# Kernel tuning notes

Measured on AMD Instinct MI355X. Metric: run time of the kernel, lower is better.

Reference implementation:

```python
import jax, jax.numpy as jnp
import numpy as np

NF, IN_NF, N_LAYERS = 64, 196, 3
B, H, W = 1, 256, 256
P3 = [(1, 1), (1, 1)]
P1 = [(0, 0), (0, 0)]


def conv2d(x, w, pad):
    return jax.lax.conv_general_dilated(x, w, (1, 1), pad,
                                        dimension_numbers=('NCHW', 'OIHW', 'NCHW'))


def prelu(x, a):
    return jnp.where(x >= 0, x, a[None, :, None, None] * x)


def warp(x, flow):
    # standard backward bilinear warp, zero padding outside the image
    Bx, C, Hx, Wx = x.shape
    yy, xx = jnp.meshgrid(jnp.arange(Hx, dtype=x.dtype),
                          jnp.arange(Wx, dtype=x.dtype), indexing='ij')
    px = xx[None] + flow[:, 0]  # (B,H,W)
    py = yy[None] + flow[:, 1]

    def sample(img, px, py):  # img (C,H,W); px,py (H,W)
        x0 = jnp.floor(px)
        y0 = jnp.floor(py)
        x1 = x0 + 1.0
        y1 = y0 + 1.0
        wx1 = px - x0
        wx0 = 1.0 - wx1
        wy1 = py - y0
        wy0 = 1.0 - wy1

        def gather(xi, yi):
            valid = (xi >= 0) & (xi <= Wx - 1) & (yi >= 0) & (yi <= Hx - 1)
            xc = jnp.clip(xi, 0, Wx - 1).astype(jnp.int32)
            yc = jnp.clip(yi, 0, Hx - 1).astype(jnp.int32)
            return img[:, yc, xc] * valid.astype(img.dtype)

        return (gather(x0, y0) * (wx0 * wy0) + gather(x1, y0) * (wx1 * wy0)
                + gather(x0, y1) * (wx0 * wy1) + gather(x1, y1) * (wx1 * wy1))

    return jax.vmap(sample)(x, px, py)


def setup_inputs() -> dict:
    key = jax.random.key(0)
    ks = jax.random.split(key, 11)
    s = 0.05
    return {
        'feat_0': jax.random.normal(ks[0], (B, 64, H, W), jnp.float32),
        'feat_1': jax.random.normal(ks[1], (B, 64, H, W), jnp.float32),
        'feat_dense': jax.random.normal(ks[2], (B, 64, H, W), jnp.float32),
        'flow': jax.random.normal(ks[3], (B, 4, H, W), jnp.float32),
        'space_mask': jax.random.uniform(ks[4], (B, 1, H, W), jnp.float32),
        'head_w': jax.random.normal(ks[5], (IN_NF, IN_NF, 3, 3), jnp.float32) * s,
        'head_a': jnp.full((IN_NF,), 0.25, jnp.float32),
        'conv_w': jax.random.normal(ks[6], (N_LAYERS, IN_NF, IN_NF, 3, 3), jnp.float32) * s,
        'conv_a': jnp.full((N_LAYERS, IN_NF), 0.25, jnp.float32),
        'last_w': jax.random.normal(ks[7], (4 + NF, IN_NF * (N_LAYERS + 1), 1, 1), jnp.float32) * s,
        'last_b': jax.random.normal(ks[8], (4 + NF,), jnp.float32) * s,
        'mask_w': jax.random.normal(ks[9], (2, NF, 3, 3), jnp.float32) * s,
        'mask_b': jax.random.normal(ks[10], (2,), jnp.float32) * s,
    }


def reference(feat_0, feat_1, feat_dense, flow, space_mask,
              head_w, head_a, conv_w, conv_a, last_w, last_b, mask_w, mask_b):
    f0 = warp(feat_0, flow[:, :2])
    f1 = warp(feat_1, flow[:, 2:4])
    x = jnp.concatenate([f0, f1, feat_dense, flow], axis=1)  # (B, in_nf, H, W)
    sm_up = jnp.repeat(jnp.repeat(space_mask, 2, axis=2), 2, axis=3)

    # head: conv3x3 -> PReLU, then mask (dense / use_sparsity=False path)
    x = prelu(conv2d(x, head_w, P3), head_a) * space_mask
    outs = [x]
    for i in range(N_LAYERS):
        x = conv2d(x, conv_w[i], P3) * space_mask
        x = prelu(x, conv_a[i])
        outs.append(x)
    x = conv2d(jnp.concatenate(outs, axis=1), last_w, P1) + last_b[None, :, None, None]

    smn = conv2d(x[:, 4:], mask_w, P3) + mask_b[None, :, None, None]

    Bx, Cx, Hx, Wx = x.shape
    x_up = jax.image.resize(x, (Bx, Cx, 2 * Hx, 2 * Wx), method='bilinear')
    smn_up = jax.image.resize(smn, (Bx, 2, 2 * Hx, 2 * Wx), method='bilinear')

    flow_out = x_up[:, :4]
    feat_t = x_up[:, 4:]
    # eval-mode mask (training=False): hard argmax between channel 0 and 1
    mask_next = (smn_up[:, :1] > smn_up[:, 1:2]).astype(x.dtype) * sm_up
    return flow_out, feat_t, mask_next
```

## Files before the change

kernel.cpp:

```cpp
#include <hip/hip_runtime.h>

typedef _Float16 f16;
typedef _Float16 f16x8 __attribute__((ext_vector_type(8)));
typedef _Float16 f16x4 __attribute__((ext_vector_type(4)));
typedef float    f32x4 __attribute__((ext_vector_type(4)));
typedef float    f32x16 __attribute__((ext_vector_type(16)));

#define MFMA16(a,b,c) __builtin_amdgcn_mfma_f32_16x16x32_f16(a,b,c,0,0,0)
#define MFMA32(a,b,c) __builtin_amdgcn_mfma_f32_32x32x16_f16(a,b,c,0,0,0)

#define NPIX 65536
#define PXS   8
#define KHS   2064
#define K16S  4128
#define HS    8256
#define CBS   16512
#define ROWH  115584
#define RBYTES 231168
#define SBUF  ((size_t)258*RBYTES)

#define PKSUB  7168
#define PK_CONV 903168
#define NMICRO 117

#define PKL_CB  5120
#define PKL_BI  35840

#define ASTG 14336
#define BSTG 16640

__global__ void k_pack_conv(const float* __restrict__ head_w,
                            const float* __restrict__ conv_w,
                            f16* __restrict__ dst)
{
    int t = blockIdx.x*256 + threadIdx.x;
    int lane = t & 63; t >>= 6;
    int ob  = t % 7;  t /= 7;
    int sel = t & 1;  t >>= 1;
    int kx  = t % 3;  t /= 3;
    int k16 = t & 1;  t >>= 1;
    int cb  = t % 7;  t /= 7;
    int ky  = t % 3;  t /= 3;
    int li  = t;
    if (li >= 4) return;
    if (cb == 6 && k16 == 1) return;
    const float* W = (li == 0) ? head_w : (conv_w + (size_t)(li-1)*196*196*9);
    int oc  = ob*32 + (lane & 31);
    int ic0 = cb*32 + k16*16 + (lane >> 5)*8;
    int tap = ky*3 + kx;
    f16x8 v;
#pragma unroll
    for (int j = 0; j < 8; ++j) {
        int ic = ic0 + j;
        float x = 0.f;
        if (oc < 196 && ic < 196) x = W[((size_t)oc*196 + ic)*9 + tap];
        f16 h = (f16)x;
        v[j] = (sel == 0) ? h : (f16)(x - (float)h);
    }
    int pos = ky*39 + ((cb < 6) ? (cb*6 + k16*3 + kx) : (36 + kx));
    *(f16x8*)(dst + (size_t)li*PK_CONV + (size_t)pos*PKSUB
              + (size_t)(sel*7 + ob)*512 + (size_t)lane*8) = v;
}

__global__ void k_pack_last(const float* __restrict__ last_w, f16* __restrict__ dst)
{
    int t = blockIdx.x*256 + threadIdx.x;
    if (t >= 4*7*5*2*64) return;
    int lane = t & 63; t >>= 6;
    int sel  = t & 1;  t >>= 1;
    int ob   = t % 5;  t /= 5;
    int cb   = t % 7;  t /= 7;
    int bi   = t;
    int oc = ob*16 + (lane & 15);
    int k0 = cb*32 + (lane >> 4)*8;
    f16x8 v;
#pragma unroll
    for (int j = 0; j < 8; ++j) {
        int k = k0 + j;
        float x = 0.f;
        if (oc < 68 && k < 196) x = last_w[(size_t)oc*784 + bi*196 + k];
        f16 h = (f16)x;
        v[j] = (sel == 0) ? h : (f16)(x - (float)h);
    }
    *(f16x8*)(dst + (((size_t)((bi*7+cb)*5 + ob)*2 + sel)*64 + lane)*8) = v;
}

__global__ void k_zero_halo(f16* __restrict__ bufA, f16* __restrict__ bufB)
{
    int c = blockIdx.x*256 + threadIdx.x;
    int end = c & 1; c >>= 1;
    int kh  = c & 1; c >>= 1;
    int k16 = c & 1; c >>= 1;
    int h   = c & 1; c >>= 1;
    int cb  = c % 7; c /= 7;
    int row = c % 258; c /= 258;
    if (c >= 2) return;
    f16* base = (c == 0) ? bufA : bufB;
    f16* p = base + (size_t)row*ROWH + cb*CBS + h*HS + k16*K16S + kh*KHS + (end ? 257 : 0)*PXS;
    f16x8 z = {(f16)0,(f16)0,(f16)0,(f16)0,(f16)0,(f16)0,(f16)0,(f16)0};
    *(f16x8*)p = z;
}

struct Gath { int o00,o01,o10,o11; float w00,w01,w10,w11; };

__device__ inline Gath mk_gath(float pxf, float pyf)
{
    float x0 = floorf(pxf), y0 = floorf(pyf);
    float x1 = x0 + 1.f, y1 = y0 + 1.f;
    float wx1 = pxf - x0, wx0 = 1.f - wx1;
    float wy1 = pyf - y0, wy0 = 1.f - wy1;
    bool vx0 = (x0 >= 0.f) && (x0 <= 255.f);
    bool vx1 = (x1 >= 0.f) && (x1 <= 255.f);
    bool vy0 = (y0 >= 0.f) && (y0 <= 255.f);
    bool vy1 = (y1 >= 0.f) && (y1 <= 255.f);
    int ix0 = min(max((int)x0, 0), 255);
    int ix1 = min(max((int)x1, 0), 255);
    int iy0 = min(max((int)y0, 0), 255);
    int iy1 = min(max((int)y1, 0), 255);
    Gath g;
    g.o00 = iy0*256 + ix0; g.w00 = (vx0 && vy0) ? wx0*wy0 : 0.f;
    g.o01 = iy0*256 + ix1; g.w01 = (vx1 && vy0) ? wx1*wy0 : 0.f;
    g.o10 = iy1*256 + ix0; g.w10 = (vx0 && vy1) ? wx0*wy1 : 0.f;
    g.o11 = iy1*256 + ix1; g.w11 = (vx1 && vy1) ? wx1*wy1 : 0.f;
    return g;
}

__device__ inline void store4n(f16* __restrict__ rowb, int slot, int c0,
                               float a, float b, float c, float d)
{
    f16x4 hi, lo;
    f16 h;
    h = (f16)a; hi[0] = h; lo[0] = (f16)(a - (float)h);
    h = (f16)b; hi[1] = h; lo[1] = (f16)(b - (float)h);
    h = (f16)c; hi[2] = h; lo[2] = (f16)(c - (float)h);
    h = (f16)d; hi[3] = h; lo[3] = (f16)(d - (float)h);
    int cb = c0 >> 5, w32 = c0 & 31;
    f16* p = rowb + cb*CBS + (w32 >> 4)*K16S + ((w32 >> 3) & 1)*KHS
                 + (size_t)slot*PXS + (w32 & 7);
    *(f16x4*)p        = hi;
    *(f16x4*)(p + HS) = lo;
}

__global__ void k_warp_concat(const float* __restrict__ f0, const float* __restrict__ f1,
                              const float* __restrict__ fd, const float* __restrict__ flow,
                              f16* __restrict__ out)
{
    int px = blockIdx.x*256 + threadIdx.x;
    int row = px >> 8, col = px & 255;
    f16* rowb = out + (size_t)(row+1)*ROWH;
    int slot = col + 1;
    Gath g0 = mk_gath((float)col + flow[px],          (float)row + flow[NPIX   + px]);
    Gath g1 = mk_gath((float)col + flow[2*NPIX + px], (float)row + flow[3*NPIX + px]);
#pragma unroll
    for (int c = 0; c < 64; c += 4) {
        float v[4];
#pragma unroll
        for (int r = 0; r < 4; ++r) {
            const float* im = f0 + (size_t)(c+r)*NPIX;
            v[r] = g0.w00*im[g0.o00] + g0.w01*im[g0.o01] + g0.w10*im[g0.o10] + g0.w11*im[g0.o11];
        }
        store4n(rowb, slot, c, v[0], v[1], v[2], v[3]);
    }
#pragma unroll
    for (int c = 0; c < 64; c += 4) {
        float v[4];
#pragma unroll
        for (int r = 0; r < 4; ++r) {
            const float* im = f1 + (size_t)(c+r)*NPIX;
            v[r] = g1.w00*im[g1.o00] + g1.w01*im[g1.o01] + g1.w10*im[g1.o10] + g1.w11*im[g1.o11];
        }
        store4n(rowb, slot, 64 + c, v[0], v[1], v[2], v[3]);
    }
#pragma unroll
    for (int c = 0; c < 64; c += 4) {
        store4n(rowb, slot, 128 + c, fd[(size_t)(c+0)*NPIX + px], fd[(size_t)(c+1)*NPIX + px],
                                     fd[(size_t)(c+2)*NPIX + px], fd[(size_t)(c+3)*NPIX + px]);
    }
    store4n(rowb, slot, 192, flow[px], flow[NPIX+px], flow[2*NPIX+px], flow[3*NPIX+px]);
#pragma unroll
    for (int c = 196; c < 224; c += 4) store4n(rowb, slot, c, 0.f, 0.f, 0.f, 0.f);
}

template<int NOB, int OB0>
__device__ __forceinline__ void micro(const char* __restrict__ ab, const char* __restrict__ bl,
                                      f32x16 (&acc)[4][2], int lane)
{
    f16x8 Bh[2], Bl[2];
    Bh[0] = *(const f16x8*)(bl);
    Bh[1] = *(const f16x8*)(bl + 512);
    Bl[0] = *(const f16x8*)(bl + 8320);
    Bl[1] = *(const f16x8*)(bl + 8320 + 512);
#pragma unroll
    for (int o = 0; o < NOB; ++o) {
        f16x8 Ah = *(const f16x8*)(ab + (OB0 + o)*1024 + lane*16);
        f16x8 Al = *(const f16x8*)(ab + (7 + OB0 + o)*1024 + lane*16);
#pragma unroll
        for (int pt = 0; pt < 2; ++pt) {
            acc[o][pt] = MFMA32(Ah, Bh[pt], acc[o][pt]);
            acc[o][pt] = MFMA32(Al, Bh[pt], acc[o][pt]);
            acc[o][pt] = MFMA32(Ah, Bl[pt], acc[o][pt]);
        }
    }
}

__global__ __launch_bounds__(256, 2)
void k_conv32(const f16* __restrict__ in, f16* __restrict__ out,
              const f16* __restrict__ pack, const float* __restrict__ alpha,
              const float* __restrict__ mask)
{
    __shared__ __align__(16) char As[3][ASTG];
    __shared__ __align__(16) char Bs[2][BSTG];

    int bid = blockIdx.x;
    int wg  = (bid & 7)*64 + (bid >> 3);
    int row  = wg >> 1;
    int half = wg & 1;
    int tid  = threadIdx.x;
    int lane = tid & 63;
    int w    = tid >> 6;
    int ocg  = ((w >> 1) ^ bid) & 1;
    int pxg  = w & 1;
    int l31 = lane & 31, lk = lane >> 5;
    int cb0 = half*128;

    f32x16 acc[4][2];
#pragma unroll
    for (int o = 0; o < 4; ++o)
#pragma unroll
        for (int pt = 0; pt < 2; ++pt)
#pragma unroll
            for (int e = 0; e < 16; ++e) acc[o][pt][e] = 0.f;

    auto stageA = [&](int b, const f16* src) {
        __builtin_amdgcn_global_load_lds(
            (const __attribute__((address_space(1))) void*)(src + (size_t)tid*8),
            (__attribute__((address_space(3))) void*)(&As[b][0] + tid*16), 16, 0, 0);
        __builtin_amdgcn_global_load_lds(
            (const __attribute__((address_space(1))) void*)(src + (size_t)(tid+256)*8),
            (__attribute__((address_space(3))) void*)(&As[b][0] + (tid+256)*16), 16, 0, 0);
        __builtin_amdgcn_global_load_lds(
            (const __attribute__((address_space(1))) void*)(src + (size_t)(tid+512)*8),
            (__attribute__((address_space(3))) void*)(&As[b][0] + (tid+512)*16), 16, 0, 0);
        if (tid < 128)
            __builtin_amdgcn_global_load_lds(
                (const __attribute__((address_space(1))) void*)(src + (size_t)(tid+768)*8),
                (__attribute__((address_space(3))) void*)(&As[b][0] + (tid+768)*16), 16, 0, 0);
    };

    auto stageB = [&](int b, const f16* g) {
#pragma unroll
        for (int u = 0; u < 5; ++u) {
            int c = tid + u*256;
            if (u < 4 || c < 1040) {
                int pl = c / 130;
                int i  = c - pl*130;
                const f16* src = g + (size_t)pl*KHS + (size_t)(cb0 + i)*PXS;
                __builtin_amdgcn_global_load_lds(
                    (const __attribute__((address_space(1))) void*)src,
                    (__attribute__((address_space(3))) void*)(&Bs[b][0] + c*16),
                    16, 0, 0);
            }
        }
    };

    const int lbase = lk*2080 + (pxg*64 + l31)*16;

    const f16* g = in + (size_t)row*ROWH;
    stageB(0, g);
    stageA(0, pack);
    stageA(1, pack + PKSUB);
    __syncthreads();

    int bsel = 0;
    int q = 0;
    for (int ky = 0; ky < 3; ++ky) {
        for (int cb = 0; cb < 7; ++cb) {
            int nk16 = (cb == 6) ? 1 : 2;
            bool lastPhase = (ky == 2) && (cb == 6);
            if (!lastPhase) {
                const f16* gn = (cb < 6) ? (g + CBS) : (g + ROWH - 6*CBS);
                stageB(bsel ^ 1, gn);
                g = gn;
            }
            for (int k16 = 0; k16 < nk16; ++k16) {
#pragma unroll
                for (int kx = 0; kx < 3; ++kx) {
                    if (q + 2 < NMICRO) {
                        int nb = q + 2;
                        stageA(nb - (nb/3)*3, pack + (size_t)nb*PKSUB);
                    }
                    const char* ab = &As[q - (q/3)*3][0];
                    const char* bl = &Bs[bsel][0] + lbase + k16*4160 + kx*16;
                    __builtin_amdgcn_s_setprio(1);
                    if (ocg == 0) micro<4,0>(ab, bl, acc, lane);
                    else          micro<3,4>(ab, bl, acc, lane);
                    __builtin_amdgcn_s_setprio(0);
                    __syncthreads();
                    ++q;
                }
            }
            bsel ^= 1;
        }
    }

    int nob = (ocg == 0) ? 4 : 3;
    int ob0 = (ocg == 0) ? 0 : 4;
    int colbase = cb0 + pxg*64;
    float mv[2];
#pragma unroll
    for (int pt = 0; pt < 2; ++pt) mv[pt] = mask[row*256 + colbase + pt*32 + l31];
#pragma unroll
    for (int o = 0; o < 4; ++o) {
        if (o >= nob) continue;
        int ob = ob0 + o;
#pragma unroll
        for (int qg = 0; qg < 4; ++qg) {
            int oc0 = ob*32 + 8*qg + 4*lk;
            f32x4 a4 = *(const f32x4*)(alpha + min(oc0, 192));
#pragma unroll
            for (int pt = 0; pt < 2; ++pt) {
                f16x4 hi, lo;
#pragma unroll
                for (int e = 0; e < 4; ++e) {
                    float v = acc[o][pt][qg*4 + e];
                    v = (v >= 0.f ? v : a4[e]*v) * mv[pt];
                    f16 h = (f16)v;
                    hi[e] = h;
                    lo[e] = (f16)(v - (float)h);
                }
                f16* p = out + (size_t)(row+1)*ROWH + (size_t)(colbase + pt*32 + l31 + 1)*PXS
                       + lk*4 + ob*CBS + (qg >> 1)*K16S + (qg & 1)*KHS;
                *(f16x4*)p        = hi;
                *(f16x4*)(p + HS) = lo;
            }
        }
    }
}

__global__ __launch_bounds__(256, 4)
void k_acc_last(const f16* __restrict__ in, const f16* __restrict__ pack,
                const float* __restrict__ bias, float* __restrict__ accp, int bi)
{
    int lane = threadIdx.x & 63;
    int wid  = (blockIdx.x << 2) | (threadIdx.x >> 6);
    int row  = wid >> 3;
    int col0 = (wid & 7) << 5;
    int l15 = lane & 15, lk = lane >> 4;

    f32x4 acc[5][2];
#pragma unroll
    for (int i = 0; i < 5; ++i)
#pragma unroll
        for (int j = 0; j < 2; ++j)
            acc[i][j] = (f32x4){0.f, 0.f, 0.f, 0.f};

    const f16* bb = in + (size_t)(row+1)*ROWH + (size_t)(col0 + l15 + 1)*PXS
                  + (lk >> 1)*K16S + (lk & 1)*KHS;
    const f16* ap = pack + (size_t)bi*PKL_BI + (size_t)lane*8;
    for (int cb = 0; cb < 7; ++cb) {
        f16x8 bh[2], bl[2];
#pragma unroll
        for (int pb = 0; pb < 2; ++pb) {
            const f16* p = bb + cb*CBS + pb*16*PXS;
            bh[pb] = *(const f16x8*)p;
            bl[pb] = *(const f16x8*)(p + HS);
        }
        const f16* a = ap + cb*PKL_CB;
#pragma unroll
        for (int ob = 0; ob < 5; ++ob) {
            f16x8 ah = *(const f16x8*)(a + ob*1024);
            f16x8 al = *(const f16x8*)(a + ob*1024 + 512);
#pragma unroll
            for (int pb = 0; pb < 2; ++pb) {
                acc[ob][pb] = MFMA16(ah, bh[pb], acc[ob][pb]);
                acc[ob][pb] = MFMA16(ah, bl[pb], acc[ob][pb]);
                acc[ob][pb] = MFMA16(al, bh[pb], acc[ob][pb]);
            }
        }
    }
#pragma unroll
    for (int ob = 0; ob < 5; ++ob) {
        int oc0 = ob*16 + lk*4;
        if (oc0 >= 72) continue;
#pragma unroll
        for (int pb = 0; pb < 2; ++pb) {
            int px = row*256 + col0 + pb*16 + l15;
            float* dst = accp + (size_t)px*72 + oc0;
            f32x4 d = acc[ob][pb];
            if (bi == 0) {
                f32x4 b4;
#pragma unroll
                for (int r = 0; r < 4; ++r) b4[r] = bias[min(oc0 + r, 67)];
                *(f32x4*)dst = d + b4;
            } else {
                *(f32x4*)dst = *(const f32x4*)dst + d;
            }
        }
    }
}

__global__ void k_smn(const float* __restrict__ accp, const float* __restrict__ mw,
                      const float* __restrict__ mb, float* __restrict__ smn)
{
    int px = blockIdx.x*256 + threadIdx.x;
    int row = px >> 8, col = px & 255;
    float s0 = mb[0], s1 = mb[1];
    for (int ky = 0; ky < 3; ++ky) {
        int r = row + ky - 1;
        if ((unsigned)r > 255u) continue;
        for (int kx = 0; kx < 3; ++kx) {
            int c = col + kx - 1;
            if ((unsigned)c > 255u) continue;
            const float* ab = accp + ((size_t)r*256 + c)*72 + 4;
            const float* w  = mw + ky*3 + kx;
#pragma unroll
            for (int ch = 0; ch < 64; ch += 4) {
                f32x4 v = *(const f32x4*)(ab + ch);
                s0 += v[0]*w[(ch+0)*9] + v[1]*w[(ch+1)*9] + v[2]*w[(ch+2)*9] + v[3]*w[(ch+3)*9];
                s1 += v[0]*w[(64+ch+0)*9] + v[1]*w[(64+ch+1)*9] + v[2]*w[(64+ch+2)*9] + v[3]*w[(64+ch+3)*9];
            }
        }
    }
    smn[px]        = s0;
    smn[NPIX + px] = s1;
}

__global__ void k_upsample(const float* __restrict__ accp, float* __restrict__ outp)
{
    int o = blockIdx.x*256 + threadIdx.x;
    int oy = o >> 9, ox = o & 511;
    int my = oy >> 1, mx = ox >> 1;
    int r0, r1, c0, c1; float wy0, wy1, wx0, wx1;
    if (oy & 1) { r0 = my;            r1 = min(my+1, 255); wy0 = 0.75f; wy1 = 0.25f; }
    else        { r0 = max(my-1, 0);  r1 = my;             wy0 = 0.25f; wy1 = 0.75f; }
    if (ox & 1) { c0 = mx;            c1 = min(mx+1, 255); wx0 = 0.75f; wx1 = 0.25f; }
    else        { c0 = max(mx-1, 0);  c1 = mx;             wx0 = 0.25f; wx1 = 0.75f; }
    const float* p00 = accp + ((size_t)r0*256 + c0)*72;
    const float* p01 = accp + ((size_t)r0*256 + c1)*72;
    const float* p10 = accp + ((size_t)r1*256 + c0)*72;
    const float* p11 = accp + ((size_t)r1*256 + c1)*72;
    float w00 = wy0*wx0, w01 = wy0*wx1, w10 = wy1*wx0, w11 = wy1*wx1;
#pragma unroll
    for (int ch = 0; ch < 68; ch += 4) {
        f32x4 va = *(const f32x4*)(p00 + ch);
        f32x4 vb = *(const f32x4*)(p01 + ch);
        f32x4 vc = *(const f32x4*)(p10 + ch);
        f32x4 vd = *(const f32x4*)(p11 + ch);
        f32x4 v;
#pragma unroll
        for (int r = 0; r < 4; ++r)
            v[r] = w00*va[r] + w01*vb[r] + w10*vc[r] + w11*vd[r];
        outp[(size_t)(ch+0)*262144 + o] = v[0];
        outp[(size_t)(ch+1)*262144 + o] = v[1];
        outp[(size_t)(ch+2)*262144 + o] = v[2];
        outp[(size_t)(ch+3)*262144 + o] = v[3];
    }
}

__global__ void k_mask(const float* __restrict__ smn, const float* __restrict__ sm,
                       float* __restrict__ outp)
{
    int o = blockIdx.x*256 + threadIdx.x;
    int oy = o >> 9, ox = o & 511;
    int my = oy >> 1, mx = ox >> 1;
    int r0, r1, c0, c1; float wy0, wy1, wx0, wx1;
    if (oy & 1) { r0 = my;            r1 = min(my+1, 255); wy0 = 0.75f; wy1 = 0.25f; }
    else        { r0 = max(my-1, 0);  r1 = my;             wy0 = 0.25f; wy1 = 0.75f; }
    if (ox & 1) { c0 = mx;            c1 = min(mx+1, 255); wx0 = 0.75f; wx1 = 0.25f; }
    else        { c0 = max(mx-1, 0);  c1 = mx;             wx0 = 0.25f; wx1 = 0.75f; }
    float w00 = wy0*wx0, w01 = wy0*wx1, w10 = wy1*wx0, w11 = wy1*wx1;
    int i00 = r0*256 + c0, i01 = r0*256 + c1, i10 = r1*256 + c0, i11 = r1*256 + c1;
    float s0 = w00*smn[i00] + w01*smn[i01] + w10*smn[i10] + w11*smn[i11];
    float s1 = w00*smn[NPIX+i00] + w01*smn[NPIX+i01] + w10*smn[NPIX+i10] + w11*smn[NPIX+i11];
    outp[(size_t)68*262144 + o] = (s0 > s1) ? sm[my*256 + mx] : 0.f;
}

extern "C" void kernel_launch(void* const* d_in, const int* in_sizes, int n_in,
                              void* d_out, int out_size, void* d_ws, size_t ws_size,
                              hipStream_t stream)
{
    const float* feat0  = (const float*)d_in[0];
    const float* feat1  = (const float*)d_in[1];
    const float* featd  = (const float*)d_in[2];
    const float* flow   = (const float*)d_in[3];
    const float* smask  = (const float*)d_in[4];
    const float* head_w = (const float*)d_in[5];
    const float* head_a = (const float*)d_in[6];
    const float* conv_w = (const float*)d_in[7];
    const float* conv_a = (const float*)d_in[8];
    const float* last_w = (const float*)d_in[9];
    const float* last_b = (const float*)d_in[10];
    const float* mask_w = (const float*)d_in[11];
    const float* mask_b = (const float*)d_in[12];
    float* outp = (float*)d_out;

    char* ws = (char*)d_ws;
    size_t off = 0;
    f16* bufA = (f16*)(ws + off); off += SBUF;
    f16* bufB = (f16*)(ws + off); off += SBUF;
    f16* packc = (f16*)(ws + off); off += (size_t)4*PK_CONV*2;
    f16* packl = (f16*)(ws + off); off += (size_t)4*PKL_BI*2;
    float* accp = (float*)(ws + off); off += (size_t)NPIX*72*4;
    float* smn  = (float*)(ws + off); off += (size_t)2*NPIX*4;

    hipMemsetAsync(bufA, 0, RBYTES, stream);
    hipMemsetAsync((char*)bufA + (size_t)257*RBYTES, 0, RBYTES, stream);
    hipMemsetAsync(bufB, 0, RBYTES, stream);
    hipMemsetAsync((char*)bufB + (size_t)257*RBYTES, 0, RBYTES, stream);
    k_zero_halo<<<226, 256, 0, stream>>>(bufA, bufB);

    k_pack_conv<<<1764, 256, 0, stream>>>(head_w, conv_w, packc);
    k_pack_last<<<70, 256, 0, stream>>>(last_w, packl);
    k_warp_concat<<<256, 256, 0, stream>>>(feat0, feat1, featd, flow, bufA);

    k_conv32<<<512, 256, 0, stream>>>(bufA, bufB, packc, head_a, smask);
    k_acc_last<<<512, 256, 0, stream>>>(bufB, packl, last_b, accp, 0);
    k_conv32<<<512, 256, 0, stream>>>(bufB, bufA, packc + (size_t)1*PK_CONV, conv_a, smask);
    k_acc_last<<<512, 256, 0, stream>>>(bufA, packl, last_b, accp, 1);
    k_conv32<<<512, 256, 0, stream>>>(bufA, bufB, packc + (size_t)2*PK_CONV, conv_a + 196, smask);
    k_acc_last<<<512, 256, 0, stream>>>(bufB, packl, last_b, accp, 2);
    k_conv32<<<512, 256, 0, stream>>>(bufB, bufA, packc + (size_t)3*PK_CONV, conv_a + 392, smask);
    k_acc_last<<<512, 256, 0, stream>>>(bufA, packl, last_b, accp, 3);

    k_smn<<<256, 256, 0, stream>>>(accp, mask_w, mask_b, smn);
    k_upsample<<<1024, 256, 0, stream>>>(accp, outp);
    k_mask<<<1024, 256, 0, stream>>>(smn, smask, outp);
}
```

Measured before the change: 804.2 us.

## Replace per-step block barriers with vmcnt waits and per-wave staging

The conv kernel is restructured so each wave stages only the weight fragments it consumes and its own pixel slice of the input tile. It uses explicit s_waitcnt vmcnt counts plus a barrier every second micro-step instead of a full __syncthreads after every step. The weight pipeline depth drops from three stages in flight to two, and the body is templated on the output-block count. The goal is to cut barrier stalls and redundant staging, but the hand-tuned vmcnt counts and the barrier skipping risk races if the wave-to-buffer ownership assumptions are wrong.

```diff
diff --git a/kernel.cpp b/kernel.cpp
--- a/kernel.cpp
+++ b/kernel.cpp
@@ -8,6 +8,10 @@
 
 #define MFMA16(a,b,c) __builtin_amdgcn_mfma_f32_16x16x32_f16(a,b,c,0,0,0)
 #define MFMA32(a,b,c) __builtin_amdgcn_mfma_f32_32x32x16_f16(a,b,c,0,0,0)
+
+#define AS1 __attribute__((address_space(1)))
+#define AS3 __attribute__((address_space(3)))
+#define WAITVM(N) asm volatile("s_waitcnt vmcnt(" #N ")" ::: "memory")
 
 #define NPIX 65536
 #define PXS   8
@@ -27,7 +31,7 @@
 #define PKL_BI  35840
 
 #define ASTG 14336
-#define BSTG 16640
+#define BSTG 17408
 
 __global__ void k_pack_conv(const float* __restrict__ head_w,
                             const float* __restrict__ conv_w,
@@ -182,137 +186,125 @@
 }
 
 template<int NOB, int OB0>
-__device__ __forceinline__ void micro(const char* __restrict__ ab, const char* __restrict__ bl,
-                                      f32x16 (&acc)[4][2], int lane)
-{
-    f16x8 Bh[2], Bl[2];
-    Bh[0] = *(const f16x8*)(bl);
-    Bh[1] = *(const f16x8*)(bl + 512);
-    Bl[0] = *(const f16x8*)(bl + 8320);
-    Bl[1] = *(const f16x8*)(bl + 8320 + 512);
-#pragma unroll
-    for (int o = 0; o < NOB; ++o) {
-        f16x8 Ah = *(const f16x8*)(ab + (OB0 + o)*1024 + lane*16);
-        f16x8 Al = *(const f16x8*)(ab + (7 + OB0 + o)*1024 + lane*16);
-#pragma unroll
-        for (int pt = 0; pt < 2; ++pt) {
-            acc[o][pt] = MFMA32(Ah, Bh[pt], acc[o][pt]);
-            acc[o][pt] = MFMA32(Al, Bh[pt], acc[o][pt]);
-            acc[o][pt] = MFMA32(Ah, Bl[pt], acc[o][pt]);
-        }
-    }
-}
-
-__global__ __launch_bounds__(256, 2)
-void k_conv32(const f16* __restrict__ in, f16* __restrict__ out,
-              const f16* __restrict__ pack, const float* __restrict__ alpha,
-              const float* __restrict__ mask)
-{
-    __shared__ __align__(16) char As[3][ASTG];
-    __shared__ __align__(16) char Bs[2][BSTG];
-
-    int bid = blockIdx.x;
-    int wg  = (bid & 7)*64 + (bid >> 3);
-    int row  = wg >> 1;
-    int half = wg & 1;
-    int tid  = threadIdx.x;
-    int lane = tid & 63;
-    int w    = tid >> 6;
-    int ocg  = ((w >> 1) ^ bid) & 1;
-    int pxg  = w & 1;
+__device__ __forceinline__ void conv_body(
+    const f16* __restrict__ in, f16* __restrict__ out,
+    const f16* __restrict__ pack, const float* __restrict__ alpha,
+    const float* __restrict__ mask,
+    char* Asb, char* Bsb, int row, int cb0, int lane, int pxg, int bid)
+{
     int l31 = lane & 31, lk = lane >> 5;
-    int cb0 = half*128;
-
-    f32x16 acc[4][2];
-#pragma unroll
-    for (int o = 0; o < 4; ++o)
+
+    f32x16 acc[NOB][2];
+#pragma unroll
+    for (int o = 0; o < NOB; ++o)
 #pragma unroll
         for (int pt = 0; pt < 2; ++pt)
 #pragma unroll
             for (int e = 0; e < 16; ++e) acc[o][pt][e] = 0.f;
 
-    auto stageA = [&](int b, const f16* src) {
+    auto stageA = [&](int b, int qi) {
+        const f16* src = pack + (size_t)qi*PKSUB;
+        char* dst = Asb + b*ASTG;
+#pragma unroll
+        for (int j = 0; j < NOB; ++j) {
+            int fr1 = OB0 + j, fr2 = 7 + OB0 + j;
+            __builtin_amdgcn_global_load_lds(
+                (const AS1 void*)(src + fr1*512 + lane*8),
+                (AS3 void*)(dst + fr1*1024 + lane*16), 16, 0, 0);
+            __builtin_amdgcn_global_load_lds(
+                (const AS1 void*)(src + fr2*512 + lane*8),
+                (AS3 void*)(dst + fr2*1024 + lane*16), 16, 0, 0);
+        }
+    };
+
+    auto stageB = [&](int b, const f16* g) {
+        char* dst = Bsb + b*BSTG;
+#pragma unroll
+        for (int u = 0; u < 8; ++u) {
+            __builtin_amdgcn_global_load_lds(
+                (const AS1 void*)(g + (size_t)u*KHS + (size_t)(cb0 + pxg*64 + lane)*PXS),
+                (AS3 void*)(dst + (u*128 + pxg*64)*16 + lane*16), 16, 0, 0);
+        }
+        int idx = lane & 15;
+        int pl  = idx >> 1;
+        int il  = idx & 1;
         __builtin_amdgcn_global_load_lds(
-            (const __attribute__((address_space(1))) void*)(src + (size_t)tid*8),
-            (__attribute__((address_space(3))) void*)(&As[b][0] + tid*16), 16, 0, 0);
-        __builtin_amdgcn_global_load_lds(
-            (const __attribute__((address_space(1))) void*)(src + (size_t)(tid+256)*8),
-            (__attribute__((address_space(3))) void*)(&As[b][0] + (tid+256)*16), 16, 0, 0);
-        __builtin_amdgcn_global_load_lds(
-            (const __attribute__((address_space(1))) void*)(src + (size_t)(tid+512)*8),
-            (__attribute__((address_space(3))) void*)(&As[b][0] + (tid+512)*16), 16, 0, 0);
-        if (tid < 128)
-            __builtin_amdgcn_global_load_lds(
-                (const __attribute__((address_space(1))) void*)(src + (size_t)(tid+768)*8),
-                (__attribute__((address_space(3))) void*)(&As[b][0] + (tid+768)*16), 16, 0, 0);
+            (const AS1 void*)(g + (size_t)pl*KHS + (size_t)(cb0 + 128 + il)*PXS),
+            (AS3 void*)(dst + 16384 + lane*16), 16, 0, 0);
     };
 
-    auto stageB = [&](int b, const f16* g) {
-#pragma unroll
-        for (int u = 0; u < 5; ++u) {
-            int c = tid + u*256;
-            if (u < 4 || c < 1040) {
-                int pl = c / 130;
-                int i  = c - pl*130;
-                const f16* src = g + (size_t)pl*KHS + (size_t)(cb0 + i)*PXS;
-                __builtin_amdgcn_global_load_lds(
-                    (const __attribute__((address_space(1))) void*)src,
-                    (__attribute__((address_space(3))) void*)(&Bs[b][0] + c*16),
-                    16, 0, 0);
-            }
-        }
+    auto bptr = [&](const char* Bb, int pl, int sl) -> const char* {
+        return (sl < 128) ? (Bb + pl*2048 + sl*16)
+                          : (Bb + 16384 + pl*32 + (sl - 128)*16);
     };
-
-    const int lbase = lk*2080 + (pxg*64 + l31)*16;
 
     const f16* g = in + (size_t)row*ROWH;
     stageB(0, g);
-    stageA(0, pack);
-    stageA(1, pack + PKSUB);
-    __syncthreads();
-
-    int bsel = 0;
-    int q = 0;
+    stageA(0, 0);
+
+    int acur = 0, bsel = 0, q = 0;
     for (int ky = 0; ky < 3; ++ky) {
         for (int cb = 0; cb < 7; ++cb) {
+            bool lastPhase = (ky == 2) && (cb == 6);
             int nk16 = (cb == 6) ? 1 : 2;
-            bool lastPhase = (ky == 2) && (cb == 6);
-            if (!lastPhase) {
-                const f16* gn = (cb < 6) ? (g + CBS) : (g + ROWH - 6*CBS);
-                stageB(bsel ^ 1, gn);
-                g = gn;
-            }
-            for (int k16 = 0; k16 < nk16; ++k16) {
+            const f16* gn = (cb < 6) ? (g + CBS) : (g + ROWH - 6*CBS);
+            for (int k16 = 0; k16 < 2; ++k16) {
+                if (k16 >= nk16) break;
 #pragma unroll
                 for (int kx = 0; kx < 3; ++kx) {
-                    if (q + 2 < NMICRO) {
-                        int nb = q + 2;
-                        stageA(nb - (nb/3)*3, pack + (size_t)nb*PKSUB);
+                    int anx = (acur == 2) ? 0 : (acur + 1);
+                    bool aload = (q + 1 < NMICRO);
+                    if (aload) stageA(anx, q + 1);
+                    if (aload) {
+                        if (k16 == 0 && kx == 1 && !lastPhase) {
+                            if (NOB == 4) WAITVM(17); else WAITVM(15);
+                        } else {
+                            if (NOB == 4) WAITVM(8);  else WAITVM(6);
+                        }
+                    } else {
+                        WAITVM(0);
                     }
-                    const char* ab = &As[q - (q/3)*3][0];
-                    const char* bl = &Bs[bsel][0] + lbase + k16*4160 + kx*16;
+                    if ((q & 1) == 0) __builtin_amdgcn_s_barrier();
+                    if (k16 == 0 && kx == 0 && !lastPhase) stageB(bsel ^ 1, gn);
+
+                    const char* ab = Asb + acur*ASTG;
+                    const char* Bb = Bsb + bsel*BSTG;
+                    f16x8 Bh[2], Bl[2];
+#pragma unroll
+                    for (int pt = 0; pt < 2; ++pt) {
+                        int sl = pxg*64 + l31 + kx + pt*32;
+                        int plh = k16*2 + lk;
+                        Bh[pt] = *(const f16x8*)bptr(Bb, plh, sl);
+                        Bl[pt] = *(const f16x8*)bptr(Bb, 4 + plh, sl);
+                    }
                     __builtin_amdgcn_s_setprio(1);
-                    if (ocg == 0) micro<4,0>(ab, bl, acc, lane);
-                    else          micro<3,4>(ab, bl, acc, lane);
+#pragma unroll
+                    for (int o = 0; o < NOB; ++o) {
+                        f16x8 Ah = *(const f16x8*)(ab + (OB0 + o)*1024 + lane*16);
+                        f16x8 Al = *(const f16x8*)(ab + (7 + OB0 + o)*1024 + lane*16);
+#pragma unroll
+                        for (int pt = 0; pt < 2; ++pt) {
+                            acc[o][pt] = MFMA32(Ah, Bh[pt], acc[o][pt]);
+                            acc[o][pt] = MFMA32(Al, Bh[pt], acc[o][pt]);
+                            acc[o][pt] = MFMA32(Ah, Bl[pt], acc[o][pt]);
+                        }
+                    }
                     __builtin_amdgcn_s_setprio(0);
-                    __syncthreads();
+                    acur = anx;
                     ++q;
                 }
             }
-            bsel ^= 1;
-        }
-    }
-
-    int nob = (ocg == 0) ? 4 : 3;
-    int ob0 = (ocg == 0) ? 0 : 4;
+            if (!lastPhase) { g = gn; bsel ^= 1; }
+        }
+    }
+
     int colbase = cb0 + pxg*64;
     float mv[2];
 #pragma unroll
     for (int pt = 0; pt < 2; ++pt) mv[pt] = mask[row*256 + colbase + pt*32 + l31];
 #pragma unroll
-    for (int o = 0; o < 4; ++o) {
-        if (o >= nob) continue;
-        int ob = ob0 + o;
+    for (int o = 0; o < NOB; ++o) {
+        int ob = OB0 + o;
 #pragma unroll
         for (int qg = 0; qg < 4; ++qg) {
             int oc0 = ob*32 + 8*qg + 4*lk;
@@ -335,6 +327,31 @@
             }
         }
     }
+}
+
+__global__ __launch_bounds__(256, 2)
+void k_conv32(const f16* __restrict__ in, f16* __restrict__ out,
+              const f16* __restrict__ pack, const float* __restrict__ alpha,
+              const float* __restrict__ mask)
+{
+    __shared__ __align__(16) char As[3][ASTG];
+    __shared__ __align__(16) char Bs[2][BSTG];
+
+    int bid = blockIdx.x;
+    int wg  = (bid & 7)*64 + (bid >> 3);
+    int row  = wg >> 1;
+    int half = wg & 1;
+    int tid  = threadIdx.x;
+    int lane = tid & 63;
+    int w    = tid >> 6;
+    int ocg  = ((w >> 1) ^ bid) & 1;
+    int pxg  = w & 1;
+    int cb0 = half*128;
+
+    if (ocg == 0)
+        conv_body<4,0>(in, out, pack, alpha, mask, &As[0][0], &Bs[0][0], row, cb0, lane, pxg, bid);
+    else
+        conv_body<3,4>(in, out, pack, alpha, mask, &As[0][0], &Bs[0][0], row, cb0, lane, pxg, bid);
 }
 
 __global__ __launch_bounds__(256, 4)
```

Result: slower. 834.3 us (+3.7%).
